# Kernel tuning notes

Measured on AMD Instinct MI355X. Metric: run time of the kernel, lower is better.

Reference implementation:

```python
import jax, jax.numpy as jnp
import numpy as np

PASS, MAP, STEP = 0, 1, 2
B, D, S, V = 64, 256, 1024, 1024  # batch, d_model, num_symbols(=2*num_keys), num_values
GRAPH_STEPS = 3


def _mlp2(x, w1, b1, w2, b2):
    # torch nn.Sequential(Linear, GELU, Linear); exact (erf) GELU
    return jax.nn.gelu(x @ w1 + b1, approximate=False) @ w2 + b2


def setup_inputs() -> dict:
    key = jax.random.key(0)
    ks = jax.random.split(key, 32)
    n = lambda k, shape, s=0.02: jax.random.normal(k, shape, jnp.float32) * s
    inp = {
        'map_memory': jnp.zeros((B, S, V), jnp.float32),
        'step_memory': jnp.zeros((B, S, S), jnp.float32),
        'event_marker': jax.random.randint(ks[0], (B,), 0, 3),
        'source_idx': jax.random.randint(ks[1], (B,), 0, S),
        'source_valid': jnp.ones((B,), bool),
        'target_symbol_idx': jax.random.randint(ks[2], (B,), 0, S),
        'target_symbol_valid': jnp.ones((B,), bool),
        'target_value_idx': jax.random.randint(ks[3], (B,), 0, V),
        'target_value_valid': jnp.ones((B,), bool),
        'evidence': n(ks[4], (B, D), 1.0),
        'query_idx': jax.random.randint(ks[5], (B,), 0, S),
        'query_valid': jnp.ones((B,), jnp.float32),
        'sym_emb': n(ks[6], (S, D)),
        'val_emb': n(ks[7], (V, D)),
        'mg_w1': n(ks[8], (D, D)), 'mg_b1': jnp.zeros((D,)),
        'mg_w2': n(ks[9], (D, 1)), 'mg_b2': jnp.zeros((1,)),
        'sg_w1': n(ks[10], (D, D)), 'sg_b1': jnp.zeros((D,)),
        'sg_w2': n(ks[11], (D, 1)), 'sg_b2': jnp.zeros((1,)),
        'sf_w1': n(ks[12], (2 * D, D)), 'sf_b1': jnp.zeros((D,)),
        'sf_w2': n(ks[13], (D, D)), 'sf_b2': jnp.zeros((D,)),
        'oh_w1': n(ks[14], (2 * D, D)), 'oh_b1': jnp.zeros((D,)),
        'oh_w2': n(ks[15], (D, V)), 'oh_b2': jnp.zeros((V,)),
    }
    return inp


def reference(map_memory, step_memory, event_marker, source_idx, source_valid,
              target_symbol_idx, target_symbol_valid, target_value_idx,
              target_value_valid, evidence, query_idx, query_valid,
              sym_emb, val_emb,
              mg_w1, mg_b1, mg_w2, mg_b2, sg_w1, sg_b1, sg_w2, sg_b2,
              sf_w1, sf_b1, sf_w2, sf_b2, oh_w1, oh_b1, oh_w2, oh_b2):
    bs = event_marker.shape[0]
    src = jnp.clip(source_idx, 0, S - 1)
    tsym = jnp.clip(target_symbol_idx, 0, S - 1)
    tval = jnp.clip(target_value_idx, 0, V - 1)

    map_gain = jax.nn.sigmoid(_mlp2(evidence, mg_w1, mg_b1, mg_w2, mg_b2))[:, 0]
    step_gain = jax.nn.sigmoid(_mlp2(evidence, sg_w1, sg_b1, sg_w2, sg_b2))[:, 0]

    map_mask = ((event_marker == PASS) | (event_marker == MAP)) & source_valid & target_value_valid
    step_mask = (event_marker == STEP) & source_valid & target_symbol_valid

    # one-hot outer-product update == single-entry scatter-add per batch element
    b = jnp.arange(bs)
    map_memory = map_memory.at[b, src, tval].add(map_gain * map_mask.astype(map_gain.dtype))
    step_memory = step_memory.at[b, src, tsym].add(step_gain * step_mask.astype(step_gain.dtype))

    # query readout: 3-step batched graph walk
    qi = jnp.clip(query_idx, 0, S - 1)
    walk = jax.nn.one_hot(qi, S, dtype=jnp.float32) * query_valid[:, None]
    acc_values = jnp.einsum('bs,bsv->bv', walk, map_memory)
    acc_symbols = walk @ sym_emb  # symbol bank is shared across batch
    for _ in range(GRAPH_STEPS):
        walk = jnp.einsum('bs,bst->bt', walk, step_memory)
        acc_values = acc_values + jnp.einsum('bs,bsv->bv', walk, map_memory)
        acc_symbols = acc_symbols + walk @ sym_emb
    graph_value_vec = acc_values @ val_emb  # bv,vd->bd
    graph_state = jnp.concatenate([acc_symbols, graph_value_vec], axis=-1)
    logits = _mlp2(graph_state, oh_w1, oh_b1, oh_w2, oh_b2)
    feedback = _mlp2(graph_state, sf_w1, sf_b1, sf_w2, sf_b2)
    return logits, feedback
```

## Files before the change

kernel.cpp:

```cpp
#include <hip/hip_runtime.h>
#include <cmath>

#define BSZ 64
#define DD  256
#define SS  1024
#define VV  1024

__device__ __forceinline__ float gelu_exact(float x) {
    return 0.5f * x * (1.0f + erff(x * 0.70710678118654752440f));
}
__device__ __forceinline__ float sigmoidf(float x) {
    return 1.0f / (1.0f + expf(-x));
}

__device__ int compact_nnz(const float* vec, int* nnz,
                           int* wave_cnt, int* wave_off, int* total_p)
{
    int tid = threadIdx.x;
    bool p = (vec[tid] != 0.0f);
    unsigned long long m = __ballot(p ? 1 : 0);
    int lane = tid & 63, wid = tid >> 6;
    if (lane == 0) wave_cnt[wid] = (int)__popcll(m);
    __syncthreads();
    if (tid == 0) {
        int o = 0;
        for (int w = 0; w < 16; ++w) { wave_off[w] = o; o += wave_cnt[w]; }
        *total_p = o;
    }
    __syncthreads();
    if (p) nnz[wave_off[wid] + (int)__popcll(m & ((1ULL << lane) - 1ULL))] = tid;
    __syncthreads();
    return *total_p;
}

__global__ __launch_bounds__(1024) void fused_kernel(
    const float* __restrict__ map_mem, const float* __restrict__ step_mem,
    const int* __restrict__ event_marker, const int* __restrict__ source_idx,
    const int* __restrict__ tsym_idx, const int* __restrict__ tval_idx,
    const int* __restrict__ query_idx, const float* __restrict__ query_valid,
    const float* __restrict__ evidence, const float* __restrict__ sym_emb,
    const float* __restrict__ val_emb,
    const float* __restrict__ mg_w1, const float* __restrict__ mg_b1,
    const float* __restrict__ mg_w2, const float* __restrict__ mg_b2,
    const float* __restrict__ sg_w1, const float* __restrict__ sg_b1,
    const float* __restrict__ sg_w2, const float* __restrict__ sg_b2,
    const float* __restrict__ sf_w1, const float* __restrict__ sf_b1,
    const float* __restrict__ sf_w2, const float* __restrict__ sf_b2,
    const float* __restrict__ oh_w1, const float* __restrict__ oh_b1,
    const float* __restrict__ oh_w2, const float* __restrict__ oh_b2,
    float* __restrict__ out)
{
    int b   = blockIdx.x & 63;
    int j   = blockIdx.x >> 6;
    int tid = threadIdx.x;

    __shared__ float ev[DD];
    __shared__ __attribute__((aligned(16))) float part[4096];
    __shared__ float wcur[SS];
    __shared__ float wsum[SS];
    __shared__ int   nnz[SS];
    __shared__ int   wave_cnt[16], wave_off[16], total;
    __shared__ float gsh[2 * DD];
    __shared__ float h1s[DD];
    __shared__ float redw[4];
    __shared__ float gg[2];

    int   em   = event_marker[b];
    int   src  = min(max(source_idx[b], 0), SS - 1);
    int   tsym = min(max(tsym_idx[b], 0), SS - 1);
    int   tval = min(max(tval_idx[b], 0), VV - 1);
    int   qi   = min(max(query_idx[b], 0), SS - 1);
    float qv   = query_valid[b];

    const float* stepb = step_mem + (size_t)b * SS * SS;
    const float* mapb  = map_mem  + (size_t)b * SS * VV;

    float rowqi = stepb[(size_t)qi * SS + tid];

    if (tid < DD) ev[tid] = evidence[b * DD + tid];
    __syncthreads();

    bool use_map = (em == 0 || em == 1);
    {
        const float* w1 = use_map ? mg_w1 : sg_w1;
        int cg = tid & 63, kp = tid >> 6;
        float a0 = 0.f, a1 = 0.f, a2 = 0.f, a3 = 0.f;
        #pragma unroll 4
        for (int k = kp * 16; k < kp * 16 + 16; ++k) {
            float4 w = *(const float4*)(w1 + (size_t)k * DD + 4 * cg);
            float e = ev[k];
            a0 = fmaf(e, w.x, a0); a1 = fmaf(e, w.y, a1);
            a2 = fmaf(e, w.z, a2); a3 = fmaf(e, w.w, a3);
        }
        *(float4*)&part[kp * 256 + 4 * cg] = make_float4(a0, a1, a2, a3);
    }
    __syncthreads();
    if (tid < 256) {
        const float* b1g = use_map ? mg_b1 : sg_b1;
        const float* w2g = use_map ? mg_w2 : sg_w2;
        float s = 0.f;
        #pragma unroll
        for (int kp = 0; kp < 16; ++kp) s += part[kp * 256 + tid];
        float hh = gelu_exact(s + b1g[tid]);
        float r = hh * w2g[tid];
        #pragma unroll
        for (int s2 = 32; s2; s2 >>= 1) r += __shfl_xor(r, s2);
        if ((tid & 63) == 0) redw[tid >> 6] = r;
    }
    __syncthreads();
    if (tid == 0) {
        float g = sigmoidf(redw[0] + redw[1] + redw[2] + redw[3] +
                           (use_map ? mg_b2[0] : sg_b2[0]));
        gg[0] = use_map ? g : 0.f;
        gg[1] = (em == 2) ? g : 0.f;
    }
    __syncthreads();
    float gmap = gg[0], gstep = gg[1];

    float w1v = qv * (rowqi + ((qi == src && tid == tsym) ? gstep : 0.0f));
    wcur[tid] = w1v;
    wsum[tid] = ((tid == qi) ? qv : 0.0f) + w1v;
    __syncthreads();

    for (int it = 0; it < 2; ++it) {
        int tot = compact_nnz(wcur, nnz, wave_cnt, wave_off, &total);
        float acc = 0.0f;
        for (int i = 0; i < tot; ++i) {
            int s = nnz[i];
            acc = fmaf(wcur[s], stepb[(size_t)s * SS + tid], acc);
        }
        acc += (tid == tsym) ? wcur[src] * gstep : 0.0f;
        __syncthreads();
        wcur[tid] = acc;
        wsum[tid] += acc;
        __syncthreads();
    }

    int tot = compact_nnz(wsum, nnz, wave_cnt, wave_off, &total);
    float av = 0.0f;
    for (int i = 0; i < tot; ++i) {
        int s = nnz[i];
        av = fmaf(wsum[s], mapb[(size_t)s * VV + tid], av);
    }
    av += (tid == tval) ? wsum[src] * gmap : 0.0f;

    float asym = 0.0f;
    if (tid < DD) {
        for (int i = 0; i < tot; ++i) {
            int s = nnz[i];
            asym = fmaf(wsum[s], sym_emb[s * DD + tid], asym);
        }
    }
    __syncthreads();
    wcur[tid] = av;
    __syncthreads();
    int totv = compact_nnz(wcur, nnz, wave_cnt, wave_off, &total);
    if (tid < DD) {
        float gvd = 0.0f;
        for (int i = 0; i < totv; ++i) {
            int v = nnz[i];
            gvd = fmaf(wcur[v], val_emb[v * DD + tid], gvd);
        }
        gsh[tid]      = asym;
        gsh[DD + tid] = gvd;
    }
    __syncthreads();

    {
        const float* hw1 = j ? oh_w1 : sf_w1;
        int cg = tid & 63, kp = tid >> 6;
        float a0 = 0.f, a1 = 0.f, a2 = 0.f, a3 = 0.f;
        #pragma unroll 4
        for (int k = kp * 32; k < kp * 32 + 32; ++k) {
            float4 w = *(const float4*)(hw1 + (size_t)k * DD + 4 * cg);
            float g = gsh[k];
            a0 = fmaf(g, w.x, a0); a1 = fmaf(g, w.y, a1);
            a2 = fmaf(g, w.z, a2); a3 = fmaf(g, w.w, a3);
        }
        *(float4*)&part[kp * 256 + 4 * cg] = make_float4(a0, a1, a2, a3);
    }
    __syncthreads();
    if (tid < 256) {
        const float* hb1 = j ? oh_b1 : sf_b1;
        float s = 0.f;
        #pragma unroll
        for (int kp = 0; kp < 16; ++kp) s += part[kp * 256 + tid];
        h1s[tid] = gelu_exact(s + hb1[tid]);
    }
    __syncthreads();

    if (j == 0) {
        int cg = tid & 63, kp = tid >> 6;
        float a0 = 0.f, a1 = 0.f, a2 = 0.f, a3 = 0.f;
        #pragma unroll 4
        for (int k = kp * 16; k < kp * 16 + 16; ++k) {
            float4 w = *(const float4*)(sf_w2 + (size_t)k * DD + 4 * cg);
            float h = h1s[k];
            a0 = fmaf(h, w.x, a0); a1 = fmaf(h, w.y, a1);
            a2 = fmaf(h, w.z, a2); a3 = fmaf(h, w.w, a3);
        }
        *(float4*)&part[kp * 256 + 4 * cg] = make_float4(a0, a1, a2, a3);
        __syncthreads();
        if (tid < 256) {
            float s = 0.f;
            #pragma unroll
            for (int kp2 = 0; kp2 < 16; ++kp2) s += part[kp2 * 256 + tid];
            out[(size_t)BSZ * VV + (size_t)b * DD + tid] = sf_b2[tid] + s;
        }
    } else {
        int cbase = (j - 1) * 512;
        int cg = tid & 127, kp = tid >> 7;
        float a0 = 0.f, a1 = 0.f, a2 = 0.f, a3 = 0.f;
        #pragma unroll 4
        for (int k = kp * 32; k < kp * 32 + 32; ++k) {
            float4 w = *(const float4*)(oh_w2 + (size_t)k * VV + cbase + 4 * cg);
            float h = h1s[k];
            a0 = fmaf(h, w.x, a0); a1 = fmaf(h, w.y, a1);
            a2 = fmaf(h, w.z, a2); a3 = fmaf(h, w.w, a3);
        }
        *(float4*)&part[kp * 512 + 4 * cg] = make_float4(a0, a1, a2, a3);
        __syncthreads();
        if (tid < 512) {
            float s = 0.f;
            #pragma unroll
            for (int kp2 = 0; kp2 < 8; ++kp2) s += part[kp2 * 512 + tid];
            out[(size_t)b * VV + cbase + tid] = oh_b2[cbase + tid] + s;
        }
    }
}

extern "C" void kernel_launch(void* const* d_in, const int* in_sizes, int n_in,
                              void* d_out, int out_size, void* d_ws, size_t ws_size,
                              hipStream_t stream)
{
    const float* map_mem      = (const float*)d_in[0];
    const float* step_mem     = (const float*)d_in[1];
    const int*   event_marker = (const int*)  d_in[2];
    const int*   source_idx   = (const int*)  d_in[3];
    const int*   tsym_idx     = (const int*)  d_in[5];
    const int*   tval_idx     = (const int*)  d_in[7];
    const float* evidence     = (const float*)d_in[9];
    const int*   query_idx    = (const int*)  d_in[10];
    const float* query_valid  = (const float*)d_in[11];
    const float* sym_emb      = (const float*)d_in[12];
    const float* val_emb      = (const float*)d_in[13];
    const float* mg_w1 = (const float*)d_in[14];
    const float* mg_b1 = (const float*)d_in[15];
    const float* mg_w2 = (const float*)d_in[16];
    const float* mg_b2 = (const float*)d_in[17];
    const float* sg_w1 = (const float*)d_in[18];
    const float* sg_b1 = (const float*)d_in[19];
    const float* sg_w2 = (const float*)d_in[20];
    const float* sg_b2 = (const float*)d_in[21];
    const float* sf_w1 = (const float*)d_in[22];
    const float* sf_b1 = (const float*)d_in[23];
    const float* sf_w2 = (const float*)d_in[24];
    const float* sf_b2 = (const float*)d_in[25];
    const float* oh_w1 = (const float*)d_in[26];
    const float* oh_b1 = (const float*)d_in[27];
    const float* oh_w2 = (const float*)d_in[28];
    const float* oh_b2 = (const float*)d_in[29];

    fused_kernel<<<192, 1024, 0, stream>>>(map_mem, step_mem,
        event_marker, source_idx, tsym_idx, tval_idx, query_idx, query_valid,
        evidence, sym_emb, val_emb,
        mg_w1, mg_b1, mg_w2, mg_b2, sg_w1, sg_b1, sg_w2, sg_b2,
        sf_w1, sf_b1, sf_w2, sf_b2, oh_w1, oh_b1, oh_w2, oh_b2,
        (float*)d_out);
}
```

Measured before the change: 19.95 us.

## Skip unused gain MLPs and pair batches in logits blocks to reuse weights

The gate MLPs now run only when their gain can actually reach the output (the source row is touched by the walk), so for sparse memories the evidence MLP is mostly skipped. Logits blocks now each handle two batch elements and a 256-column slice, so each oh_w1/oh_w2 weight load feeds two batches. The compaction prefix sum is computed redundantly per thread to drop one barrier. The cost is that each logits block repeats the full graph walk for two batches, which may lengthen the critical path.

```diff
diff --git a/kernel.cpp b/kernel.cpp
--- a/kernel.cpp
+++ b/kernel.cpp
@@ -6,6 +6,29 @@
 #define SS  1024
 #define VV  1024
 
+struct Ptrs {
+    const float *map_mem, *step_mem;
+    const int *em, *src, *tsym, *tval, *qidx;
+    const float *qvalid, *evidence, *sym_emb, *val_emb;
+    const float *mg_w1, *mg_b1, *mg_w2, *mg_b2;
+    const float *sg_w1, *sg_b1, *sg_w2, *sg_b2;
+    const float *sf_w1, *sf_b1, *sf_w2, *sf_b2;
+    const float *oh_w1, *oh_b1, *oh_w2, *oh_b2;
+};
+
+struct __align__(16) Shmem {
+    float part[8192];
+    float wcur[SS];
+    float wsum[SS];
+    int   nnz[SS];
+    int   wave_cnt[16];
+    float gsh[2][2 * DD];
+    float h1s[2][DD];
+    float ev[DD];
+    float redw[4];
+    float ggv;
+};
+
 __device__ __forceinline__ float gelu_exact(float x) {
     return 0.5f * x * (1.0f + erff(x * 0.70710678118654752440f));
 }
@@ -13,218 +36,256 @@
     return 1.0f / (1.0f + expf(-x));
 }
 
-__device__ int compact_nnz(const float* vec, int* nnz,
-                           int* wave_cnt, int* wave_off, int* total_p)
+__device__ int compact_nnz(Shmem& sm, const float* vec)
 {
     int tid = threadIdx.x;
-    bool p = (vec[tid] != 0.0f);
-    unsigned long long m = __ballot(p ? 1 : 0);
+    bool pnz = (vec[tid] != 0.0f);
+    unsigned long long m = __ballot(pnz ? 1 : 0);
     int lane = tid & 63, wid = tid >> 6;
-    if (lane == 0) wave_cnt[wid] = (int)__popcll(m);
-    __syncthreads();
-    if (tid == 0) {
-        int o = 0;
-        for (int w = 0; w < 16; ++w) { wave_off[w] = o; o += wave_cnt[w]; }
-        *total_p = o;
-    }
-    __syncthreads();
-    if (p) nnz[wave_off[wid] + (int)__popcll(m & ((1ULL << lane) - 1ULL))] = tid;
-    __syncthreads();
-    return *total_p;
-}
-
-__global__ __launch_bounds__(1024) void fused_kernel(
-    const float* __restrict__ map_mem, const float* __restrict__ step_mem,
-    const int* __restrict__ event_marker, const int* __restrict__ source_idx,
-    const int* __restrict__ tsym_idx, const int* __restrict__ tval_idx,
-    const int* __restrict__ query_idx, const float* __restrict__ query_valid,
-    const float* __restrict__ evidence, const float* __restrict__ sym_emb,
-    const float* __restrict__ val_emb,
-    const float* __restrict__ mg_w1, const float* __restrict__ mg_b1,
-    const float* __restrict__ mg_w2, const float* __restrict__ mg_b2,
-    const float* __restrict__ sg_w1, const float* __restrict__ sg_b1,
-    const float* __restrict__ sg_w2, const float* __restrict__ sg_b2,
-    const float* __restrict__ sf_w1, const float* __restrict__ sf_b1,
-    const float* __restrict__ sf_w2, const float* __restrict__ sf_b2,
-    const float* __restrict__ oh_w1, const float* __restrict__ oh_b1,
-    const float* __restrict__ oh_w2, const float* __restrict__ oh_b2,
-    float* __restrict__ out)
-{
-    int b   = blockIdx.x & 63;
-    int j   = blockIdx.x >> 6;
+    if (lane == 0) sm.wave_cnt[wid] = (int)__popcll(m);
+    __syncthreads();
+    int off = 0, tot = 0;
+    #pragma unroll
+    for (int w = 0; w < 16; ++w) {
+        int c = sm.wave_cnt[w];
+        off += (w < wid) ? c : 0;
+        tot += c;
+    }
+    if (pnz) sm.nnz[off + (int)__popcll(m & ((1ULL << lane) - 1ULL))] = tid;
+    __syncthreads();
+    return tot;
+}
+
+__device__ float gains_mlp(Shmem& sm, const float* __restrict__ w1,
+                           const float* __restrict__ b1,
+                           const float* __restrict__ w2, float b2v,
+                           const float* __restrict__ evb)
+{
     int tid = threadIdx.x;
-
-    __shared__ float ev[DD];
-    __shared__ __attribute__((aligned(16))) float part[4096];
-    __shared__ float wcur[SS];
-    __shared__ float wsum[SS];
-    __shared__ int   nnz[SS];
-    __shared__ int   wave_cnt[16], wave_off[16], total;
-    __shared__ float gsh[2 * DD];
-    __shared__ float h1s[DD];
-    __shared__ float redw[4];
-    __shared__ float gg[2];
-
-    int   em   = event_marker[b];
-    int   src  = min(max(source_idx[b], 0), SS - 1);
-    int   tsym = min(max(tsym_idx[b], 0), SS - 1);
-    int   tval = min(max(tval_idx[b], 0), VV - 1);
-    int   qi   = min(max(query_idx[b], 0), SS - 1);
-    float qv   = query_valid[b];
-
-    const float* stepb = step_mem + (size_t)b * SS * SS;
-    const float* mapb  = map_mem  + (size_t)b * SS * VV;
-
-    float rowqi = stepb[(size_t)qi * SS + tid];
-
-    if (tid < DD) ev[tid] = evidence[b * DD + tid];
-    __syncthreads();
-
-    bool use_map = (em == 0 || em == 1);
-    {
-        const float* w1 = use_map ? mg_w1 : sg_w1;
-        int cg = tid & 63, kp = tid >> 6;
-        float a0 = 0.f, a1 = 0.f, a2 = 0.f, a3 = 0.f;
-        #pragma unroll 4
-        for (int k = kp * 16; k < kp * 16 + 16; ++k) {
-            float4 w = *(const float4*)(w1 + (size_t)k * DD + 4 * cg);
-            float e = ev[k];
-            a0 = fmaf(e, w.x, a0); a1 = fmaf(e, w.y, a1);
-            a2 = fmaf(e, w.z, a2); a3 = fmaf(e, w.w, a3);
-        }
-        *(float4*)&part[kp * 256 + 4 * cg] = make_float4(a0, a1, a2, a3);
-    }
+    if (tid < DD) sm.ev[tid] = evb[tid];
+    __syncthreads();
+    int cg = tid & 63, kp = tid >> 6;
+    float a0 = 0.f, a1 = 0.f, a2 = 0.f, a3 = 0.f;
+    #pragma unroll 4
+    for (int k = kp * 16; k < kp * 16 + 16; ++k) {
+        float4 w = *(const float4*)(w1 + (size_t)k * DD + 4 * cg);
+        float e = sm.ev[k];
+        a0 = fmaf(e, w.x, a0); a1 = fmaf(e, w.y, a1);
+        a2 = fmaf(e, w.z, a2); a3 = fmaf(e, w.w, a3);
+    }
+    *(float4*)&sm.part[kp * 256 + 4 * cg] = make_float4(a0, a1, a2, a3);
     __syncthreads();
     if (tid < 256) {
-        const float* b1g = use_map ? mg_b1 : sg_b1;
-        const float* w2g = use_map ? mg_w2 : sg_w2;
         float s = 0.f;
         #pragma unroll
-        for (int kp = 0; kp < 16; ++kp) s += part[kp * 256 + tid];
-        float hh = gelu_exact(s + b1g[tid]);
-        float r = hh * w2g[tid];
+        for (int p = 0; p < 16; ++p) s += sm.part[p * 256 + tid];
+        float hh = gelu_exact(s + b1[tid]);
+        float r = hh * w2[tid];
         #pragma unroll
         for (int s2 = 32; s2; s2 >>= 1) r += __shfl_xor(r, s2);
-        if ((tid & 63) == 0) redw[tid >> 6] = r;
-    }
-    __syncthreads();
-    if (tid == 0) {
-        float g = sigmoidf(redw[0] + redw[1] + redw[2] + redw[3] +
-                           (use_map ? mg_b2[0] : sg_b2[0]));
-        gg[0] = use_map ? g : 0.f;
-        gg[1] = (em == 2) ? g : 0.f;
-    }
-    __syncthreads();
-    float gmap = gg[0], gstep = gg[1];
-
-    float w1v = qv * (rowqi + ((qi == src && tid == tsym) ? gstep : 0.0f));
-    wcur[tid] = w1v;
-    wsum[tid] = ((tid == qi) ? qv : 0.0f) + w1v;
+        if ((tid & 63) == 0) sm.redw[tid >> 6] = r;
+    }
+    __syncthreads();
+    if (tid == 0)
+        sm.ggv = sigmoidf(sm.redw[0] + sm.redw[1] + sm.redw[2] + sm.redw[3] + b2v);
+    __syncthreads();
+    return sm.ggv;
+}
+
+__device__ void walk_one(Shmem& sm, const Ptrs& p, int b, float rowqi,
+                         float* gshrow)
+{
+    int tid = threadIdx.x;
+    int   em   = p.em[b];
+    int   src  = min(max(p.src[b],  0), SS - 1);
+    int   tsym = min(max(p.tsym[b], 0), SS - 1);
+    int   tval = min(max(p.tval[b], 0), VV - 1);
+    int   qi   = min(max(p.qidx[b], 0), SS - 1);
+    float qv   = p.qvalid[b];
+    bool em2 = (em == 2), emM = (em == 0 || em == 1);
+
+    const float* stepb = p.step_mem + (size_t)b * SS * SS;
+    const float* mapb  = p.map_mem  + (size_t)b * SS * VV;
+    const float* evb   = p.evidence + (size_t)b * DD;
+
+    float gstep = 0.f;
+    bool gdone = false;
+    if (em2 && qv != 0.f && qi == src) {
+        gstep = gains_mlp(sm, p.sg_w1, p.sg_b1, p.sg_w2, p.sg_b2[0], evb);
+        gdone = true;
+    }
+
+    sm.wcur[tid] = qv * (rowqi + ((qi == src && tid == tsym) ? gstep : 0.f));
+    sm.wsum[tid] = ((tid == qi) ? qv : 0.f) + sm.wcur[tid];
     __syncthreads();
 
     for (int it = 0; it < 2; ++it) {
-        int tot = compact_nnz(wcur, nnz, wave_cnt, wave_off, &total);
+        int tot = compact_nnz(sm, sm.wcur);
+        float srcv = sm.wcur[src];
+        if (em2 && !gdone && srcv != 0.f) {
+            gstep = gains_mlp(sm, p.sg_w1, p.sg_b1, p.sg_w2, p.sg_b2[0], evb);
+            gdone = true;
+        }
         float acc = 0.0f;
         for (int i = 0; i < tot; ++i) {
-            int s = nnz[i];
-            acc = fmaf(wcur[s], stepb[(size_t)s * SS + tid], acc);
-        }
-        acc += (tid == tsym) ? wcur[src] * gstep : 0.0f;
-        __syncthreads();
-        wcur[tid] = acc;
-        wsum[tid] += acc;
-        __syncthreads();
-    }
-
-    int tot = compact_nnz(wsum, nnz, wave_cnt, wave_off, &total);
+            int s = sm.nnz[i];
+            acc = fmaf(sm.wcur[s], stepb[(size_t)s * SS + tid], acc);
+        }
+        acc += (tid == tsym) ? srcv * gstep : 0.0f;
+        __syncthreads();
+        sm.wcur[tid] = acc;
+        sm.wsum[tid] += acc;
+        __syncthreads();
+    }
+
+    int tot = compact_nnz(sm, sm.wsum);
+    float wsrc = sm.wsum[src];
+    float gmap = 0.f;
+    if (emM && wsrc != 0.f)
+        gmap = gains_mlp(sm, p.mg_w1, p.mg_b1, p.mg_w2, p.mg_b2[0], evb);
+
     float av = 0.0f;
     for (int i = 0; i < tot; ++i) {
-        int s = nnz[i];
-        av = fmaf(wsum[s], mapb[(size_t)s * VV + tid], av);
-    }
-    av += (tid == tval) ? wsum[src] * gmap : 0.0f;
+        int s = sm.nnz[i];
+        av = fmaf(sm.wsum[s], mapb[(size_t)s * VV + tid], av);
+    }
+    av += (tid == tval) ? wsrc * gmap : 0.0f;
 
     float asym = 0.0f;
     if (tid < DD) {
         for (int i = 0; i < tot; ++i) {
-            int s = nnz[i];
-            asym = fmaf(wsum[s], sym_emb[s * DD + tid], asym);
-        }
-    }
-    __syncthreads();
-    wcur[tid] = av;
-    __syncthreads();
-    int totv = compact_nnz(wcur, nnz, wave_cnt, wave_off, &total);
+            int s = sm.nnz[i];
+            asym = fmaf(sm.wsum[s], p.sym_emb[s * DD + tid], asym);
+        }
+    }
+    __syncthreads();
+    sm.wcur[tid] = av;
+    __syncthreads();
+    int totv = compact_nnz(sm, sm.wcur);
     if (tid < DD) {
         float gvd = 0.0f;
         for (int i = 0; i < totv; ++i) {
-            int v = nnz[i];
-            gvd = fmaf(wcur[v], val_emb[v * DD + tid], gvd);
-        }
-        gsh[tid]      = asym;
-        gsh[DD + tid] = gvd;
-    }
-    __syncthreads();
-
-    {
-        const float* hw1 = j ? oh_w1 : sf_w1;
-        int cg = tid & 63, kp = tid >> 6;
-        float a0 = 0.f, a1 = 0.f, a2 = 0.f, a3 = 0.f;
-        #pragma unroll 4
-        for (int k = kp * 32; k < kp * 32 + 32; ++k) {
-            float4 w = *(const float4*)(hw1 + (size_t)k * DD + 4 * cg);
-            float g = gsh[k];
-            a0 = fmaf(g, w.x, a0); a1 = fmaf(g, w.y, a1);
-            a2 = fmaf(g, w.z, a2); a3 = fmaf(g, w.w, a3);
-        }
-        *(float4*)&part[kp * 256 + 4 * cg] = make_float4(a0, a1, a2, a3);
-    }
-    __syncthreads();
-    if (tid < 256) {
-        const float* hb1 = j ? oh_b1 : sf_b1;
-        float s = 0.f;
-        #pragma unroll
-        for (int kp = 0; kp < 16; ++kp) s += part[kp * 256 + tid];
-        h1s[tid] = gelu_exact(s + hb1[tid]);
-    }
-    __syncthreads();
-
-    if (j == 0) {
-        int cg = tid & 63, kp = tid >> 6;
-        float a0 = 0.f, a1 = 0.f, a2 = 0.f, a3 = 0.f;
-        #pragma unroll 4
-        for (int k = kp * 16; k < kp * 16 + 16; ++k) {
-            float4 w = *(const float4*)(sf_w2 + (size_t)k * DD + 4 * cg);
-            float h = h1s[k];
-            a0 = fmaf(h, w.x, a0); a1 = fmaf(h, w.y, a1);
-            a2 = fmaf(h, w.z, a2); a3 = fmaf(h, w.w, a3);
-        }
-        *(float4*)&part[kp * 256 + 4 * cg] = make_float4(a0, a1, a2, a3);
+            int v = sm.nnz[i];
+            gvd = fmaf(sm.wcur[v], p.val_emb[v * DD + tid], gvd);
+        }
+        gshrow[tid]      = asym;
+        gshrow[DD + tid] = gvd;
+    }
+    __syncthreads();
+}
+
+__global__ __launch_bounds__(1024) void fused_kernel(Ptrs p,
+                                                     float* __restrict__ out)
+{
+    __shared__ Shmem sm;
+    int bid = blockIdx.x, tid = threadIdx.x;
+
+    if (bid < 64) {
+        int b = bid;
+        int qi = min(max(p.qidx[b], 0), SS - 1);
+        float rowqi = p.step_mem[(size_t)b * SS * SS + (size_t)qi * SS + tid];
+        walk_one(sm, p, b, rowqi, sm.gsh[0]);
+
+        {
+            int cg = tid & 63, kp = tid >> 6;
+            float a0 = 0.f, a1 = 0.f, a2 = 0.f, a3 = 0.f;
+            #pragma unroll 4
+            for (int k = kp * 32; k < kp * 32 + 32; ++k) {
+                float4 w = *(const float4*)(p.sf_w1 + (size_t)k * DD + 4 * cg);
+                float g = sm.gsh[0][k];
+                a0 = fmaf(g, w.x, a0); a1 = fmaf(g, w.y, a1);
+                a2 = fmaf(g, w.z, a2); a3 = fmaf(g, w.w, a3);
+            }
+            *(float4*)&sm.part[kp * 256 + 4 * cg] = make_float4(a0, a1, a2, a3);
+        }
         __syncthreads();
         if (tid < 256) {
             float s = 0.f;
             #pragma unroll
-            for (int kp2 = 0; kp2 < 16; ++kp2) s += part[kp2 * 256 + tid];
-            out[(size_t)BSZ * VV + (size_t)b * DD + tid] = sf_b2[tid] + s;
-        }
-    } else {
-        int cbase = (j - 1) * 512;
-        int cg = tid & 127, kp = tid >> 7;
-        float a0 = 0.f, a1 = 0.f, a2 = 0.f, a3 = 0.f;
-        #pragma unroll 4
-        for (int k = kp * 32; k < kp * 32 + 32; ++k) {
-            float4 w = *(const float4*)(oh_w2 + (size_t)k * VV + cbase + 4 * cg);
-            float h = h1s[k];
-            a0 = fmaf(h, w.x, a0); a1 = fmaf(h, w.y, a1);
-            a2 = fmaf(h, w.z, a2); a3 = fmaf(h, w.w, a3);
-        }
-        *(float4*)&part[kp * 512 + 4 * cg] = make_float4(a0, a1, a2, a3);
-        __syncthreads();
-        if (tid < 512) {
+            for (int pp = 0; pp < 16; ++pp) s += sm.part[pp * 256 + tid];
+            sm.h1s[0][tid] = gelu_exact(s + p.sf_b1[tid]);
+        }
+        __syncthreads();
+
+        {
+            int cg = tid & 63, kp = tid >> 6;
+            float a0 = 0.f, a1 = 0.f, a2 = 0.f, a3 = 0.f;
+            #pragma unroll 4
+            for (int k = kp * 16; k < kp * 16 + 16; ++k) {
+                float4 w = *(const float4*)(p.sf_w2 + (size_t)k * DD + 4 * cg);
+                float h = sm.h1s[0][k];
+                a0 = fmaf(h, w.x, a0); a1 = fmaf(h, w.y, a1);
+                a2 = fmaf(h, w.z, a2); a3 = fmaf(h, w.w, a3);
+            }
+            *(float4*)&sm.part[kp * 256 + 4 * cg] = make_float4(a0, a1, a2, a3);
+        }
+        __syncthreads();
+        if (tid < 256) {
             float s = 0.f;
             #pragma unroll
-            for (int kp2 = 0; kp2 < 8; ++kp2) s += part[kp2 * 512 + tid];
-            out[(size_t)b * VV + cbase + tid] = oh_b2[cbase + tid] + s;
+            for (int pp = 0; pp < 16; ++pp) s += sm.part[pp * 256 + tid];
+            out[(size_t)BSZ * VV + (size_t)b * DD + tid] = p.sf_b2[tid] + s;
+        }
+    } else {
+        int idx = bid - 64, pair = idx >> 2, q = idx & 3;
+        int b0 = pair * 2, b1 = b0 + 1, c0 = q * 256;
+
+        int qi0 = min(max(p.qidx[b0], 0), SS - 1);
+        int qi1 = min(max(p.qidx[b1], 0), SS - 1);
+        float rq0 = p.step_mem[(size_t)b0 * SS * SS + (size_t)qi0 * SS + tid];
+        float rq1 = p.step_mem[(size_t)b1 * SS * SS + (size_t)qi1 * SS + tid];
+        walk_one(sm, p, b0, rq0, sm.gsh[0]);
+        walk_one(sm, p, b1, rq1, sm.gsh[1]);
+
+        {
+            int cg = tid & 63, kp = tid >> 6;
+            float x0 = 0.f, x1 = 0.f, x2 = 0.f, x3 = 0.f;
+            float y0 = 0.f, y1 = 0.f, y2 = 0.f, y3 = 0.f;
+            #pragma unroll 4
+            for (int k = kp * 32; k < kp * 32 + 32; ++k) {
+                float4 w = *(const float4*)(p.oh_w1 + (size_t)k * DD + 4 * cg);
+                float g0 = sm.gsh[0][k], g1 = sm.gsh[1][k];
+                x0 = fmaf(g0, w.x, x0); x1 = fmaf(g0, w.y, x1);
+                x2 = fmaf(g0, w.z, x2); x3 = fmaf(g0, w.w, x3);
+                y0 = fmaf(g1, w.x, y0); y1 = fmaf(g1, w.y, y1);
+                y2 = fmaf(g1, w.z, y2); y3 = fmaf(g1, w.w, y3);
+            }
+            *(float4*)&sm.part[kp * 256 + 4 * cg]        = make_float4(x0, x1, x2, x3);
+            *(float4*)&sm.part[4096 + kp * 256 + 4 * cg] = make_float4(y0, y1, y2, y3);
+        }
+        __syncthreads();
+        if (tid < 512) {
+            int bs = tid >> 8, c = tid & 255;
+            float s = 0.f;
+            #pragma unroll
+            for (int pp = 0; pp < 16; ++pp) s += sm.part[bs * 4096 + pp * 256 + c];
+            sm.h1s[bs][c] = gelu_exact(s + p.oh_b1[c]);
+        }
+        __syncthreads();
+
+        {
+            int cg = tid & 63, kp = tid >> 6;
+            float x0 = 0.f, x1 = 0.f, x2 = 0.f, x3 = 0.f;
+            float y0 = 0.f, y1 = 0.f, y2 = 0.f, y3 = 0.f;
+            #pragma unroll 4
+            for (int k = kp * 16; k < kp * 16 + 16; ++k) {
+                float4 w = *(const float4*)(p.oh_w2 + (size_t)k * VV + c0 + 4 * cg);
+                float h0 = sm.h1s[0][k], h1v = sm.h1s[1][k];
+                x0 = fmaf(h0, w.x, x0); x1 = fmaf(h0, w.y, x1);
+                x2 = fmaf(h0, w.z, x2); x3 = fmaf(h0, w.w, x3);
+                y0 = fmaf(h1v, w.x, y0); y1 = fmaf(h1v, w.y, y1);
+                y2 = fmaf(h1v, w.z, y2); y3 = fmaf(h1v, w.w, y3);
+            }
+            *(float4*)&sm.part[kp * 256 + 4 * cg]        = make_float4(x0, x1, x2, x3);
+            *(float4*)&sm.part[4096 + kp * 256 + 4 * cg] = make_float4(y0, y1, y2, y3);
+        }
+        __syncthreads();
+        if (tid < 512) {
+            int bs = tid >> 8, c = tid & 255;
+            float s = 0.f;
+            #pragma unroll
+            for (int pp = 0; pp < 16; ++pp) s += sm.part[bs * 4096 + pp * 256 + c];
+            out[(size_t)(b0 + bs) * VV + c0 + c] = p.oh_b2[c0 + c] + s;
         }
     }
 }
@@ -233,38 +294,26 @@
                               void* d_out, int out_size, void* d_ws, size_t ws_size,
                               hipStream_t stream)
 {
-    const float* map_mem      = (const float*)d_in[0];
-    const float* step_mem     = (const float*)d_in[1];
-    const int*   event_marker = (const int*)  d_in[2];
-    const int*   source_idx   = (const int*)  d_in[3];
-    const int*   tsym_idx     = (const int*)  d_in[5];
-    const int*   tval_idx     = (const int*)  d_in[7];
-    const float* evidence     = (const float*)d_in[9];
-    const int*   query_idx    = (const int*)  d_in[10];
-    const float* query_valid  = (const float*)d_in[11];
-    const float* sym_emb      = (const float*)d_in[12];
-    const float* val_emb      = (const float*)d_in[13];
-    const float* mg_w1 = (const float*)d_in[14];
-    const float* mg_b1 = (const float*)d_in[15];
-    const float* mg_w2 = (const float*)d_in[16];
-    const float* mg_b2 = (const float*)d_in[17];
-    const float* sg_w1 = (const float*)d_in[18];
-    const float* sg_b1 = (const float*)d_in[19];
-    const float* sg_w2 = (const float*)d_in[20];
-    const float* sg_b2 = (const float*)d_in[21];
-    const float* sf_w1 = (const float*)d_in[22];
-    const float* sf_b1 = (const float*)d_in[23];
-    const float* sf_w2 = (const float*)d_in[24];
-    const float* sf_b2 = (const float*)d_in[25];
-    const float* oh_w1 = (const float*)d_in[26];
-    const float* oh_b1 = (const float*)d_in[27];
-    const float* oh_w2 = (const float*)d_in[28];
-    const float* oh_b2 = (const float*)d_in[29];
-
-    fused_kernel<<<192, 1024, 0, stream>>>(map_mem, step_mem,
-        event_marker, source_idx, tsym_idx, tval_idx, query_idx, query_valid,
-        evidence, sym_emb, val_emb,
-        mg_w1, mg_b1, mg_w2, mg_b2, sg_w1, sg_b1, sg_w2, sg_b2,
-        sf_w1, sf_b1, sf_w2, sf_b2, oh_w1, oh_b1, oh_w2, oh_b2,
-        (float*)d_out);
-}
+    Ptrs P;
+    P.map_mem  = (const float*)d_in[0];
+    P.step_mem = (const float*)d_in[1];
+    P.em       = (const int*)  d_in[2];
+    P.src      = (const int*)  d_in[3];
+    P.tsym     = (const int*)  d_in[5];
+    P.tval     = (const int*)  d_in[7];
+    P.evidence = (const float*)d_in[9];
+    P.qidx     = (const int*)  d_in[10];
+    P.qvalid   = (const float*)d_in[11];
+    P.sym_emb  = (const float*)d_in[12];
+    P.val_emb  = (const float*)d_in[13];
+    P.mg_w1 = (const float*)d_in[14]; P.mg_b1 = (const float*)d_in[15];
+    P.mg_w2 = (const float*)d_in[16]; P.mg_b2 = (const float*)d_in[17];
+    P.sg_w1 = (const float*)d_in[18]; P.sg_b1 = (const float*)d_in[19];
+    P.sg_w2 = (const float*)d_in[20]; P.sg_b2 = (const float*)d_in[21];
+    P.sf_w1 = (const float*)d_in[22]; P.sf_b1 = (const float*)d_in[23];
+    P.sf_w2 = (const float*)d_in[24]; P.sf_b2 = (const float*)d_in[25];
+    P.oh_w1 = (const float*)d_in[26]; P.oh_b1 = (const float*)d_in[27];
+    P.oh_w2 = (const float*)d_in[28]; P.oh_b2 = (const float*)d_in[29];
+
+    fused_kernel<<<192, 1024, 0, stream>>>(P, (float*)d_out);
+}
```

Result: faster. 19.21 us (-3.7%).
